# Performance work log

Hardware: AMD Instinct MI355X
Metric: run time of the kernel (lower is better)

The kernel has to match this reference:

```python
import jax, jax.numpy as jnp
import numpy as np

EPS_DIST = 1e-7  # matches torch: log((d+1)/(d+1e-7))


def _cdist(x, p):
    # x: (B, N, D), p: (P, D) -> (B, N, P) Euclidean distances
    x2 = jnp.sum(x * x, axis=-1, keepdims=True)        # (B, N, 1)
    p2 = jnp.sum(p * p, axis=-1)                       # (P,)
    d2 = x2 + p2[None, None, :] - 2.0 * jnp.einsum('bnd,pd->bnp', x, p)
    return jnp.sqrt(jnp.maximum(d2, 1e-12))


def setup_inputs() -> dict:
    key = jax.random.key(0)
    k1, k2, k3 = jax.random.split(key, 3)
    B, C, H, W = 32, 2048, 14, 14
    num_classes, npc = 200, 10
    P = num_classes * npc
    x = jax.random.normal(k1, (B, C, H, W), dtype=jnp.float32)
    prototypes = jax.random.normal(k2, (1, P, C), dtype=jnp.float32)
    fc_w = jax.random.normal(k3, (num_classes, P), dtype=jnp.float32) * 0.02
    return {"x": x, "prototypes": prototypes, "fc_w": fc_w}


def reference(x, prototypes, fc_w):
    B, C, H, W = x.shape
    feats = x.reshape(B, C, H * W).transpose(0, 2, 1)   # (B, HW, D)
    protos = prototypes[0]                              # (P, D)
    num_classes = fc_w.shape[0]
    npc = protos.shape[0] // num_classes

    distances = _cdist(feats, protos)                   # (B, HW, P)
    similarity = jnp.log((distances + 1.0) / (distances + EPS_DIST))
    max_similarity = jnp.max(similarity, axis=1)        # (B, P)
    min_distances = jnp.min(distances, axis=1)          # (B, P)
    min_distances_per_class = min_distances.reshape(B, num_classes, npc)
    scores = max_similarity @ fc_w.T                    # (B, num_classes)
    return scores, min_distances_per_class
```

## Files before the change

### kernel.cpp

```cpp
#include <hip/hip_runtime.h>

#define INF_BITS 0x7F800000u
#define AS1 __attribute__((address_space(1)))
#define AS3 __attribute__((address_space(3)))

typedef float f32x4 __attribute__((ext_vector_type(4)));
typedef int i32x8 __attribute__((ext_vector_type(8)));
typedef unsigned int u32x2 __attribute__((ext_vector_type(2)));
typedef unsigned int u32x4 __attribute__((ext_vector_type(4)));

template <int SEL>
static __device__ __forceinline__ float dq8(unsigned int w) {
  return __builtin_amdgcn_cvt_f32_fp8((int)w, SEL);
}

__global__ __launch_bounds__(256) void k_prep_p(const float* __restrict__ protos,
                                                unsigned char* __restrict__ pTf,
                                                float* __restrict__ p2,
                                                unsigned int* __restrict__ outu) {
  const int row = blockIdx.x;
  const int tid = threadIdx.x;
  const int gi = row * 256 + tid;
  if (gi < 64000) outu[6400 + gi] = INF_BITS;
  __shared__ float red[4];
  float s = 0.f;
  unsigned int w0 = 0u, w1 = 0u;
  if (row < 2000) {
    const float* src = protos + (size_t)row * 2048 + tid * 8;
    f32x4 a = *(const f32x4*)src;
    f32x4 c = *(const f32x4*)(src + 4);
    w0 = (unsigned int)__builtin_amdgcn_cvt_pk_fp8_f32(a.x, a.y, 0, false);
    w0 = (unsigned int)__builtin_amdgcn_cvt_pk_fp8_f32(a.z, a.w, (int)w0, true);
    w1 = (unsigned int)__builtin_amdgcn_cvt_pk_fp8_f32(c.x, c.y, 0, false);
    w1 = (unsigned int)__builtin_amdgcn_cvt_pk_fp8_f32(c.z, c.w, (int)w1, true);
    float q;
    q = dq8<0>(w0); s += q * q;
    q = dq8<1>(w0); s += q * q;
    q = dq8<2>(w0); s += q * q;
    q = dq8<3>(w0); s += q * q;
    q = dq8<0>(w1); s += q * q;
    q = dq8<1>(w1); s += q * q;
    q = dq8<2>(w1); s += q * q;
    q = dq8<3>(w1); s += q * q;
  }
  *(u32x2*)(pTf + (size_t)row * 2048 + tid * 8) = (u32x2){w0, w1};
  #pragma unroll
  for (int off = 32; off; off >>= 1) s += __shfl_xor(s, off);
  if ((tid & 63) == 0) red[tid >> 6] = s;
  __syncthreads();
  if (tid == 0) p2[row] = red[0] + red[1] + red[2] + red[3];
}

__global__ __launch_bounds__(256) void k_prep_x(const float* __restrict__ x,
                                                unsigned char* __restrict__ xTf,
                                                float* __restrict__ x2p,
                                                float* __restrict__ x2) {
  const int kt = blockIdx.x;
  const int b  = blockIdx.y;
  const int tid = threadIdx.x;
  if (b == 32) {
    u32x4* pad = (u32x4*)(xTf + (size_t)6272 * 2048);
    #pragma unroll
    for (int j = tid; j < 512; j += 256)
      pad[kt * 512 + j] = (u32x4){0u, 0u, 0u, 0u};
    if (kt == 0 && tid < 128) x2[6272 + tid] = __uint_as_float(INF_BITS);
    return;
  }
  __shared__ unsigned char Ls[64][208];
  const float* src = x + ((size_t)b * 2048 + (size_t)kt * 64) * 196;
  for (int idx = tid; idx < 3136; idx += 256) {
    const int kk = idx / 49, c4 = idx - kk * 49;
    f32x4 v = *(const f32x4*)(src + (size_t)kk * 196 + c4 * 4);
    unsigned int w = (unsigned int)__builtin_amdgcn_cvt_pk_fp8_f32(v.x, v.y, 0, false);
    w = (unsigned int)__builtin_amdgcn_cvt_pk_fp8_f32(v.z, v.w, (int)w, true);
    *(unsigned int*)&Ls[kk][c4 * 4] = w;
  }
  __syncthreads();
  if (tid < 196) {
    float s = 0.f;
    #pragma unroll
    for (int j = 0; j < 64; ++j) {
      float v = dq8<0>((unsigned int)Ls[j][tid]);
      s += v * v;
    }
    x2p[kt * 6272 + b * 196 + tid] = s;
  }
  unsigned char* dstb = xTf + (size_t)b * 196 * 2048 + kt * 64;
  for (int idx = tid; idx < 784; idx += 256) {
    const int n = idx >> 2, q = idx & 3;
    const int k0 = q * 16;
    u32x4 v;
    #pragma unroll
    for (int j = 0; j < 4; ++j) {
      v[j] = (unsigned int)Ls[k0 + 4 * j + 0][n] |
             ((unsigned int)Ls[k0 + 4 * j + 1][n] << 8) |
             ((unsigned int)Ls[k0 + 4 * j + 2][n] << 16) |
             ((unsigned int)Ls[k0 + 4 * j + 3][n] << 24);
    }
    *(u32x4*)(dstb + (size_t)n * 2048 + k0) = v;
  }
}

__global__ void k_x2r(const float* __restrict__ x2p, float* __restrict__ x2) {
  int i = blockIdx.x * blockDim.x + threadIdx.x;
  if (i >= 6272) return;
  float s = 0.f;
  #pragma unroll
  for (int c = 0; c < 32; ++c) s += x2p[c * 6272 + i];
  x2[i] = s;
}

__global__ __launch_bounds__(512, 2) void k_main(
    const unsigned char* __restrict__ pTf, const unsigned char* __restrict__ xTf,
    const float* __restrict__ p2, const float* __restrict__ x2,
    unsigned int* __restrict__ outu) {
  const int orig = blockIdx.x;
  const int wgid = (orig & 7) * 50 + (orig >> 3);
  const int ptile = wgid / 50;
  const int mtile = wgid - ptile * 50;
  const int p0 = ptile * 256;
  const int m0 = mtile * 128;
  const int tid = threadIdx.x;
  const int lane = tid & 63;
  const int w = tid >> 6;
  const int wp = w >> 1;
  const int wn = w & 1;
  const int lr = lane & 15;
  const int lg = lane >> 4;

  __shared__ __align__(16) char S[98304];

  f32x4 acc[4][4];
  #pragma unroll
  for (int mi = 0; mi < 4; ++mi)
    #pragma unroll
    for (int ni = 0; ni < 4; ++ni)
      acc[mi][ni] = (f32x4){0.f, 0.f, 0.f, 0.f};

  const int rowbase = tid >> 3;
  const int chunk = (tid & 7) ^ (rowbase & 7);
  const char* gA = (const char*)pTf + (size_t)(p0 + rowbase) * 2048 + chunk * 16;
  const char* gB = (const char*)xTf + (size_t)(m0 + rowbase) * 2048 + chunk * 16;
  const int wbase = w * 1024;

#define STAGE_A(c_, kt_) do {                                                  \
    const char* s_ = gA + (size_t)(kt_) * 128;                                 \
    _Pragma("unroll")                                                          \
    for (int j_ = 0; j_ < 4; ++j_)                                             \
      __builtin_amdgcn_global_load_lds(                                        \
          (const AS1 void*)(s_ + (size_t)j_ * 64 * 2048),                      \
          (AS3 void*)(S + (c_) * 32768 + j_ * 8192 + wbase), 16, 0, 0);        \
  } while (0)
#define STAGE_B(c_, kt_) do {                                                  \
    const char* s_ = gB + (size_t)(kt_) * 128;                                 \
    _Pragma("unroll")                                                          \
    for (int j_ = 0; j_ < 2; ++j_)                                             \
      __builtin_amdgcn_global_load_lds(                                        \
          (const AS1 void*)(s_ + (size_t)j_ * 64 * 2048),                      \
          (AS3 void*)(S + 65536 + (c_) * 16384 + j_ * 8192 + wbase), 16, 0, 0);\
  } while (0)

  const int swz = ((lr & 7) << 4);
  const int koffA = (lg * 32) ^ swz;
  const int arow = (wp * 64 + lr) * 128;
  const int brow = (wn * 64 + lr) * 128;

#define READ_A1(dst_, c_, a_) do {                                             \
    const char* p_ = S + (c_) * 32768 + arow + (a_) * 2048;                    \
    u32x4 lo_ = *(const u32x4*)(p_ + koffA);                                   \
    u32x4 hi_ = *(const u32x4*)(p_ + (koffA ^ 16));                            \
    dst_ = __builtin_bit_cast(i32x8,                                           \
        __builtin_shufflevector(lo_, hi_, 0, 1, 2, 3, 4, 5, 6, 7));            \
  } while (0)
#define READ_B4(dst_, c_)                                                      \
    _Pragma("unroll")                                                          \
    for (int ni_ = 0; ni_ < 4; ++ni_) {                                        \
      const char* p_ = S + 65536 + (c_) * 16384 + brow + ni_ * 2048;           \
      u32x4 lo_ = *(const u32x4*)(p_ + koffA);                                 \
      u32x4 hi_ = *(const u32x4*)(p_ + (koffA ^ 16));                          \
      dst_[ni_] = __builtin_bit_cast(i32x8,                                    \
          __builtin_shufflevector(lo_, hi_, 0, 1, 2, 3, 4, 5, 6, 7));          \
    }

#define SCHED() __builtin_amdgcn_sched_barrier(0)
#define SBAR() do { SCHED(); __builtin_amdgcn_s_barrier(); SCHED(); } while (0)
#define LGKM0() do { asm volatile("s_waitcnt lgkmcnt(0)" ::: "memory"); SCHED(); } while (0)
#define MFMA4(mi_, af_, bf_) do { __builtin_amdgcn_s_setprio(1);               \
    _Pragma("unroll")                                                          \
    for (int ni_ = 0; ni_ < 4; ++ni_)                                          \
      acc[mi_][ni_] = __builtin_amdgcn_mfma_scale_f32_16x16x128_f8f6f4(        \
          af_, bf_[ni_], acc[mi_][ni_], 0, 0, 0, 0x7F7F7F7F, 0, 0x7F7F7F7F);   \
    __builtin_amdgcn_s_setprio(0); } while (0)

#define KT_BODY(kt_, c_, sa_, sb_, vm_, tail_) do {                            \
    if (sa_) STAGE_A((c_) ^ 1, (kt_) + 1);                                     \
    i32x8 bf[4], af0, af1;                                                     \
    READ_B4(bf, c_);                                                           \
    READ_A1(af0, c_, 0);                                                       \
    READ_A1(af1, c_, 1); MFMA4(0, af0, bf); SCHED();                           \
    READ_A1(af0, c_, 2); MFMA4(1, af1, bf); SCHED();                           \
    READ_A1(af1, c_, 3); MFMA4(2, af0, bf); SCHED();                           \
    MFMA4(3, af1, bf);                                                         \
    if (!(tail_)) {                                                            \
      LGKM0();                                                                 \
      SBAR();                                               \
      if (sb_) STAGE_B(c_, (kt_) + 2);                                         \
      if ((vm_) == 2)      asm volatile("s_waitcnt vmcnt(2)" ::: "memory");    \
      else if ((vm_) == 0) asm volatile("s_waitcnt vmcnt(0)" ::: "memory");    \
      SCHED();                                                                 \
      SBAR();                                             \
    }                                                                          \
  } while (0)

  STAGE_A(0, 0);
  STAGE_B(0, 0);
  STAGE_B(1, 1);
  asm volatile("s_waitcnt vmcnt(2)" ::: "memory");
  SCHED();
  __builtin_amdgcn_s_barrier();
  SCHED();

  #pragma unroll 1
  for (int it = 0; it < 7; ++it) {
    KT_BODY(2 * it, 0, 1, 1, 2, 0);
    KT_BODY(2 * it + 1, 1, 1, 1, 2, 0);
  }
  KT_BODY(14, 0, 1, 0, 0, 0);
  KT_BODY(15, 1, 0, 0, -1, 1);
#undef KT_BODY
#undef MFMA4
#undef READ_A1
#undef READ_B4
#undef STAGE_A
#undef STAGE_B

  const int wm_base = m0 + wn * 64;
  const int b_lo = wm_base / 196;
  int b_hi = (wm_base + 63) / 196;
  if (b_hi > 31) b_hi = 31;
  const bool wave_ok = (b_lo < 32);
  float x2v[4];
  int seg0[4];
  #pragma unroll
  for (int ni = 0; ni < 4; ++ni) {
    const int m = wm_base + ni * 16 + lr;
    x2v[ni] = x2[m];
    seg0[ni] = ((m / 196) == b_lo);
  }
  const float INF = __uint_as_float(INF_BITS);
  #pragma unroll
  for (int mi = 0; mi < 4; ++mi) {
    const int prow = p0 + wp * 64 + mi * 16 + 4 * lg;
    #pragma unroll
    for (int j = 0; j < 4; ++j) {
      const int p = prow + j;
      const float pp = p2[p];
      float ma = INF, mb = INF;
      #pragma unroll
      for (int ni = 0; ni < 4; ++ni) {
        const float d2 = x2v[ni] + pp - 2.f * acc[mi][ni][j];
        ma = fminf(ma, seg0[ni] ? d2 : INF);
        mb = fminf(mb, seg0[ni] ? INF : d2);
      }
      #pragma unroll
      for (int off = 1; off < 16; off <<= 1) {
        ma = fminf(ma, __shfl_xor(ma, off));
        mb = fminf(mb, __shfl_xor(mb, off));
      }
      if (lr == 0 && p < 2000 && wave_ok) {
        atomicMin(&outu[6400 + b_lo * 2000 + p], __float_as_uint(fmaxf(ma, 0.f)));
        if (b_hi != b_lo)
          atomicMin(&outu[6400 + b_hi * 2000 + p], __float_as_uint(fmaxf(mb, 0.f)));
      }
    }
  }
}

__global__ void k_post(float* __restrict__ out, float* __restrict__ simbuf) {
  int i = blockIdx.x * blockDim.x + threadIdx.x;
  if (i >= 64000) return;
  float d2 = out[6400 + i];
  float d = sqrtf(fmaxf(d2, 1e-12f));
  out[6400 + i] = d;
  simbuf[i] = logf((d + 1.0f) / (d + 1e-7f));
}

__global__ __launch_bounds__(256) void k_scores(const float* __restrict__ fc_w,
                                                const float* __restrict__ simbuf,
                                                float* __restrict__ out) {
  const int id = blockIdx.x * 4 + (threadIdx.x >> 6);
  const int lane = threadIdx.x & 63;
  const int b = id / 200;
  const int c = id - b * 200;
  const f32x4* sv = (const f32x4*)(simbuf + (size_t)b * 2000);
  const f32x4* wv = (const f32x4*)(fc_w + (size_t)c * 2000);
  float s = 0.f;
  #pragma unroll
  for (int it = 0; it < 8; ++it) {
    int i = lane + it * 64;
    if (i < 500) {
      f32x4 a = sv[i], w4 = wv[i];
      s += a.x * w4.x + a.y * w4.y + a.z * w4.z + a.w * w4.w;
    }
  }
  #pragma unroll
  for (int off = 32; off; off >>= 1) s += __shfl_xor(s, off);
  if (lane == 0) out[b * 200 + c] = s;
}

extern "C" void kernel_launch(void* const* d_in, const int* in_sizes, int n_in,
                              void* d_out, int out_size, void* d_ws, size_t ws_size,
                              hipStream_t stream) {
  const float* x      = (const float*)d_in[0];
  const float* protos = (const float*)d_in[1];
  const float* fc_w   = (const float*)d_in[2];
  float* out = (float*)d_out;

  char* wsb = (char*)d_ws;
  unsigned char* pTf = (unsigned char*)wsb;
  unsigned char* xTf = (unsigned char*)(wsb + 4194304);
  float* p2   = (float*)(wsb + 17301504);
  float* x2   = (float*)(wsb + 17309696);
  float* x2p  = (float*)(wsb + 17335296);
  float* simb = (float*)(wsb + 17335296);

  k_prep_p<<<2048, 256, 0, stream>>>(protos, pTf, p2, (unsigned int*)d_out);
  k_prep_x<<<dim3(32, 33), 256, 0, stream>>>(x, xTf, x2p, x2);
  k_x2r<<<25, 256, 0, stream>>>(x2p, x2);
  k_main<<<400, 512, 0, stream>>>(pTf, xTf, p2, x2, (unsigned int*)d_out);
  k_post<<<250, 256, 0, stream>>>(out, simb);
  k_scores<<<1600, 256, 0, stream>>>(fc_w, simb, out);
}
```

Measured before the change: 83.36 us.

## Triple-buffer A and B LDS stages with two-iteration-ahead prefetch

Expands shared memory to three stages for both operand tiles and issues the A and B global-to-LDS loads two k-steps ahead. It removes one barrier per iteration and fully unrolls the k loop. The aim is to hide more global load latency behind the MFMAs. LDS use rises to 144KB per workgroup, which likely prevents two workgroups per CU and so cuts occupancy.

```diff
diff --git a/kernel.cpp b/kernel.cpp
--- a/kernel.cpp
+++ b/kernel.cpp
@@ -128,7 +128,7 @@
   const int lr = lane & 15;
   const int lg = lane >> 4;
 
-  __shared__ __align__(16) char S[98304];
+  __shared__ __align__(16) char S[147456];
 
   f32x4 acc[4][4];
   #pragma unroll
@@ -157,7 +157,7 @@
     for (int j_ = 0; j_ < 2; ++j_)                                             \
       __builtin_amdgcn_global_load_lds(                                        \
           (const AS1 void*)(s_ + (size_t)j_ * 64 * 2048),                      \
-          (AS3 void*)(S + 65536 + (c_) * 16384 + j_ * 8192 + wbase), 16, 0, 0);\
+          (AS3 void*)(S + 98304 + (c_) * 16384 + j_ * 8192 + wbase), 16, 0, 0);\
   } while (0)
 
   const int swz = ((lr & 7) << 4);
@@ -175,7 +175,7 @@
 #define READ_B4(dst_, c_)                                                      \
     _Pragma("unroll")                                                          \
     for (int ni_ = 0; ni_ < 4; ++ni_) {                                        \
-      const char* p_ = S + 65536 + (c_) * 16384 + brow + ni_ * 2048;           \
+      const char* p_ = S + 98304 + (c_) * 16384 + brow + ni_ * 2048;           \
       u32x4 lo_ = *(const u32x4*)(p_ + koffA);                                 \
       u32x4 hi_ = *(const u32x4*)(p_ + (koffA ^ 16));                          \
       dst_[ni_] = __builtin_bit_cast(i32x8,                                    \
@@ -192,8 +192,8 @@
           af_, bf_[ni_], acc[mi_][ni_], 0, 0, 0, 0x7F7F7F7F, 0, 0x7F7F7F7F);   \
     __builtin_amdgcn_s_setprio(0); } while (0)
 
-#define KT_BODY(kt_, c_, sa_, sb_, vm_, tail_) do {                            \
-    if (sa_) STAGE_A((c_) ^ 1, (kt_) + 1);                                     \
+#define KT_BODY(kt_, c_, cs_, sa_, vm_, tail_) do {                            \
+    if (sa_) { STAGE_A(cs_, (kt_) + 2); STAGE_B(cs_, (kt_) + 2); }             \
     i32x8 bf[4], af0, af1;                                                     \
     READ_B4(bf, c_);                                                           \
     READ_A1(af0, c_, 0);                                                       \
@@ -203,30 +203,36 @@
     MFMA4(3, af1, bf);                                                         \
     if (!(tail_)) {                                                            \
       LGKM0();                                                                 \
-      SBAR();                                               \
-      if (sb_) STAGE_B(c_, (kt_) + 2);                                         \
-      if ((vm_) == 2)      asm volatile("s_waitcnt vmcnt(2)" ::: "memory");    \
+      if ((vm_) == 6)      asm volatile("s_waitcnt vmcnt(6)" ::: "memory");    \
       else if ((vm_) == 0) asm volatile("s_waitcnt vmcnt(0)" ::: "memory");    \
       SCHED();                                                                 \
-      SBAR();                                             \
+      SBAR();                        \
     }                                                                          \
   } while (0)
 
-  STAGE_A(0, 0);
-  STAGE_B(0, 0);
-  STAGE_B(1, 1);
-  asm volatile("s_waitcnt vmcnt(2)" ::: "memory");
+  STAGE_A(0, 0); STAGE_B(0, 0);
+  STAGE_A(1, 1); STAGE_B(1, 1);
+  asm volatile("s_waitcnt vmcnt(6)" ::: "memory");
   SCHED();
   __builtin_amdgcn_s_barrier();
   SCHED();
 
-  #pragma unroll 1
-  for (int it = 0; it < 7; ++it) {
-    KT_BODY(2 * it, 0, 1, 1, 2, 0);
-    KT_BODY(2 * it + 1, 1, 1, 1, 2, 0);
-  }
-  KT_BODY(14, 0, 1, 0, 0, 0);
-  KT_BODY(15, 1, 0, 0, -1, 1);
+  KT_BODY(0, 0, 2, 1, 6, 0);
+  KT_BODY(1, 1, 0, 1, 6, 0);
+  KT_BODY(2, 2, 1, 1, 6, 0);
+  KT_BODY(3, 0, 2, 1, 6, 0);
+  KT_BODY(4, 1, 0, 1, 6, 0);
+  KT_BODY(5, 2, 1, 1, 6, 0);
+  KT_BODY(6, 0, 2, 1, 6, 0);
+  KT_BODY(7, 1, 0, 1, 6, 0);
+  KT_BODY(8, 2, 1, 1, 6, 0);
+  KT_BODY(9, 0, 2, 1, 6, 0);
+  KT_BODY(10, 1, 0, 1, 6, 0);
+  KT_BODY(11, 2, 1, 1, 6, 0);
+  KT_BODY(12, 0, 2, 1, 6, 0);
+  KT_BODY(13, 1, 0, 1, 6, 0);
+  KT_BODY(14, 2, 0, 0, 0, 0);
+  KT_BODY(15, 0, 0, 0, -1, 1);
 #undef KT_BODY
 #undef MFMA4
 #undef READ_A1
```

Measured after the change: 187.6 us. +125.0%, slower.
